# Kernel tuning notes

Measured on AMD Instinct MI355X. Metric: run time of the kernel, lower is better.

Reference implementation:

```python
import math
import jax, jax.numpy as jnp
import numpy as np

T, D, H = 2048, 2048, 16
C = D // H
EPS = 1e-6


def _rope_tables(c, t):
    inv_freq = 1.0 / (10000.0 ** (jnp.arange(0, c, 2, dtype=jnp.float32) / c))
    freqs = jnp.arange(t, dtype=jnp.float32)[:, None] * inv_freq[None, :]  # (T, C/2)
    return jnp.sin(freqs), jnp.cos(freqs)


def _rotate_every_two(x):
    x1 = x[..., ::2]
    x2 = x[..., 1::2]
    return jnp.stack((-x2, x1), axis=-1).reshape(x.shape)


def _apply_rope(x_htc, sin, cos):
    # sin/cos: (T, C/2) -> repeat each freq twice along channel -> (1, T, C)
    sin = jnp.repeat(sin, 2, axis=-1)[None]
    cos = jnp.repeat(cos, 2, axis=-1)[None]
    return x_htc * cos + _rotate_every_two(x_htc) * sin


def _layernorm(x, w):
    mu = jnp.mean(x, axis=-1, keepdims=True)
    var = jnp.var(x, axis=-1, keepdims=True)
    return (x - mu) / jnp.sqrt(var + EPS) * w


def setup_inputs() -> dict:
    key = jax.random.key(0)
    ks = jax.random.split(key, 4)
    x = jax.random.normal(ks[0], (T, D), dtype=jnp.float32)
    W_attn = jax.random.normal(ks[1], (3 * D, D), dtype=jnp.float32) * 0.02
    b_attn = jnp.zeros((3 * D,), dtype=jnp.float32)
    W_proj = jax.random.normal(ks[2], (D, D), dtype=jnp.float32) * 0.02
    b_proj = jnp.zeros((D,), dtype=jnp.float32)
    q_ln_w = jnp.ones((C,), dtype=jnp.float32)
    k_ln_w = jnp.ones((C,), dtype=jnp.float32)
    return {"x": x, "W_attn": W_attn, "b_attn": b_attn, "W_proj": W_proj,
            "b_proj": b_proj, "q_ln_w": q_ln_w, "k_ln_w": k_ln_w}


def reference(x, W_attn, b_attn, W_proj, b_proj, q_ln_w, k_ln_w):
    t, d = x.shape
    qkv = x @ W_attn.T + b_attn                      # (T, 3D)
    q, k, v = jnp.split(qkv, 3, axis=-1)
    q = q.reshape(t, H, C).transpose(1, 0, 2)        # (H, T, C)
    k = k.reshape(t, H, C).transpose(1, 0, 2)
    v = v.reshape(t, H, C).transpose(1, 0, 2)
    q = _layernorm(q, q_ln_w)
    k = _layernorm(k, k_ln_w)
    sin, cos = _rope_tables(C, t)
    q = _apply_rope(q, sin, cos)
    k = _apply_rope(k, sin, cos)
    a = jnp.einsum("htc,hsc->hts", q, k)             # (H, T, T)
    causal = jnp.tril(jnp.ones((1, t, t))) == 0
    a = jnp.where(causal, float("-inf"), a)
    scaling = math.sqrt(C)                            # q_ln active
    a = jax.nn.softmax(a.astype(jnp.float32) / scaling, axis=-1).astype(x.dtype)
    out = jnp.einsum("hts,hsc->htc", a, v)           # (H, T, C)
    out = out.transpose(1, 0, 2).reshape(t, d)       # (T, D)
    return out @ W_proj.T + b_proj
```

## Files before the change

### kernel.cpp

```cpp
#include <hip/hip_runtime.h>
#include <hip/hip_bf16.h>
#include <math.h>

#define T_DIM 2048
#define D_DIM 2048
#define H_DIM 16
#define C_DIM 128

typedef __bf16 bf16;
typedef __attribute__((ext_vector_type(8))) __bf16 bf16x8;
typedef __attribute__((ext_vector_type(4))) __bf16 bf16x4;
typedef __attribute__((ext_vector_type(2))) __bf16 bf16x2;
typedef __attribute__((ext_vector_type(4))) float f32x4;

__device__ __forceinline__ void gload_lds16(const void* g, void* l) {
  __builtin_amdgcn_global_load_lds((__attribute__((address_space(1))) void*)g,
                                   (__attribute__((address_space(3))) void*)l,
                                   16, 0, 0);
}

__global__ __launch_bounds__(256) void cvt3(
    const float* __restrict__ x, const float* __restrict__ wa, const float* __restrict__ wp,
    bf16* __restrict__ xo, bf16* __restrict__ wao, bf16* __restrict__ wpo)
{
  const int NX = 1048576, NA = 3145728;
  int i = blockIdx.x * 256 + threadIdx.x;
  for (; i < 5242880; i += 2048 * 256) {
    const float* s; bf16* d; int off;
    if (i < NX)            { s = x;  d = xo;  off = i; }
    else if (i < NX + NA)  { s = wa; d = wao; off = i - NX; }
    else                   { s = wp; d = wpo; off = i - NX - NA; }
    float4 v = reinterpret_cast<const float4*>(s)[off];
    bf16x4 o;
    o[0] = (bf16)v.x; o[1] = (bf16)v.y; o[2] = (bf16)v.z; o[3] = (bf16)v.w;
    reinterpret_cast<bf16x4*>(d)[off] = o;
  }
}

__global__ __launch_bounds__(512, 2) void gemm384_bt_bias(
    const bf16* __restrict__ A, const bf16* __restrict__ B,
    const float* __restrict__ bias, float* __restrict__ C,
    int M, int N, int K)
{
  __shared__ __align__(16) bf16 Asl[2][128 * 64];
  __shared__ __align__(16) bf16 Bsl[2][384 * 64];
  const int tid = threadIdx.x;
  const int lane = tid & 63;
  const int wv = tid >> 6;
  const int g = lane >> 4, r16 = lane & 15;
  const int wm = wv >> 2;
  const int wn = wv & 3;

  int bid = blockIdx.x;
  int bid2 = (bid & 7) * 32 + (bid >> 3);
  const int ntn = N / 384;
  const int bn = bid2 % ntn, bm = bid2 / ntn;

  const size_t Abase = (size_t)(bm * 128) * K;
  const size_t Bbase = (size_t)(bn * 384) * K;

  f32x4 acc[2][2][2][3] = {};
  bf16x8 a0[2][2], a1[2][2];
  bf16x8 b0[3][2], b1[3][2];

  auto stageA = [&](int bb, int t) {
#pragma unroll
    for (int i = 0; i < 2; ++i) {
      int c = i * 512 + tid;
      int r = c >> 3, p = c & 7, j = p ^ (r & 7);
      gload_lds16(A + Abase + (size_t)r * K + t * 64 + j * 8,
                  (char*)&Asl[bb][0] + (size_t)c * 16);
    }
  };
  auto stageB = [&](int bb, int u, int t) {
#pragma unroll
    for (int i = 0; i < 2; ++i) {
      int c = i * 512 + tid;
      int r = c >> 3, p = c & 7, j = p ^ (r & 7);
      gload_lds16(B + Bbase + (size_t)(u * 128 + r) * K + t * 64 + j * 8,
                  (char*)&Bsl[bb][0] + u * 16384 + (size_t)c * 16);
    }
  };
  auto readAh = [&](bf16x8 (&dst)[2][2], int bufi, int qr) {
#pragma unroll
    for (int R = 0; R < 2; ++R) {
      int ar = wm * 64 + qr * 32 + R * 16 + r16;
#pragma unroll
      for (int ks = 0; ks < 2; ++ks)
        dst[R][ks] = *reinterpret_cast<const bf16x8*>(
            &Asl[bufi][ar * 64 + (((ks * 4 + g) ^ (ar & 7)) << 3)]);
    }
  };
  auto readBh = [&](bf16x8 (&dst)[3][2], int bufi, int qc) {
#pragma unroll
    for (int F = 0; F < 3; ++F) {
      int br = wn * 96 + qc * 48 + F * 16 + r16;
#pragma unroll
      for (int ks = 0; ks < 2; ++ks)
        dst[F][ks] = *reinterpret_cast<const bf16x8*>(
            &Bsl[bufi][br * 64 + (((ks * 4 + g) ^ (br & 7)) << 3)]);
    }
  };
  auto mfma12 = [&](f32x4 (&cq)[2][3], bf16x8 (&aa)[2][2], bf16x8 (&bb)[3][2]) {
    __builtin_amdgcn_s_setprio(1);
#pragma unroll
    for (int ks = 0; ks < 2; ++ks)
#pragma unroll
      for (int R = 0; R < 2; ++R)
#pragma unroll
        for (int F = 0; F < 3; ++F)
          cq[R][F] = __builtin_amdgcn_mfma_f32_16x16x32_bf16(aa[R][ks], bb[F][ks], cq[R][F], 0, 0, 0);
    __builtin_amdgcn_s_setprio(0);
  };

#define PHASESYNC()                                               \
  __builtin_amdgcn_s_barrier();                                   \
  asm volatile("s_waitcnt lgkmcnt(0)" ::: "memory");              \
  __builtin_amdgcn_sched_barrier(0);

  stageA(0, 0); stageB(0, 0, 0); stageB(0, 1, 0); stageB(0, 2, 0);
  asm volatile("s_waitcnt vmcnt(0)" ::: "memory");
  __builtin_amdgcn_s_barrier();

  const int NT = K >> 6;
  for (int t = 0; t < NT; ++t) {
    const int cb = t & 1, nb = cb ^ 1;
    const bool pf = (t + 1 < NT);
    readAh(a0, cb, 0);
    readBh(b0, cb, 0);
    if (pf) { stageA(nb, t + 1); stageB(nb, 0, t + 1); }
    PHASESYNC()
    mfma12(acc[0][0], a0, b0);
    __builtin_amdgcn_s_barrier();
    readBh(b1, cb, 1);
    if (pf) stageB(nb, 1, t + 1);
    PHASESYNC()
    mfma12(acc[0][1], a0, b1);
    __builtin_amdgcn_s_barrier();
    readAh(a1, cb, 1);
    if (pf) stageB(nb, 2, t + 1);
    PHASESYNC()
    mfma12(acc[1][1], a1, b1);
    __builtin_amdgcn_s_barrier();
    mfma12(acc[1][0], a1, b0);
    asm volatile("s_waitcnt vmcnt(0)" ::: "memory");
    __builtin_amdgcn_s_barrier();
  }
#undef PHASESYNC

#pragma unroll
  for (int qr = 0; qr < 2; ++qr)
#pragma unroll
    for (int qc = 0; qc < 2; ++qc)
#pragma unroll
      for (int R = 0; R < 2; ++R)
#pragma unroll
        for (int F = 0; F < 3; ++F) {
          int row0 = bm * 128 + wm * 64 + qr * 32 + R * 16 + g * 4;
          int col  = bn * 384 + wn * 96 + qc * 48 + F * 16 + r16;
          float bv = bias[col];
#pragma unroll
          for (int rr = 0; rr < 4; ++rr)
            C[(size_t)(row0 + rr) * N + col] = acc[qr][qc][R][F][rr] + bv;
        }
}

__global__ __launch_bounds__(256) void gemm_bt_bias(
    const bf16* __restrict__ A, const bf16* __restrict__ B,
    const float* __restrict__ bias, float* __restrict__ C,
    int M, int N, int K)
{
  __shared__ __align__(16) bf16 As[2][128 * 32];
  __shared__ __align__(16) bf16 Bs[2][128 * 32];
  const int tid = threadIdx.x;
  const int lane = tid & 63;
  const int w = tid >> 6;
  const int wm = (w >> 1) * 64, wn = (w & 1) * 64;
  const int g = lane >> 4;
  const int r16 = lane & 15;
  const int bm = blockIdx.y, bn = blockIdx.x;

  f32x4 acc[4][4] = {};

  const size_t Abase = (size_t)(bm * 128) * K;
  const size_t Bbase = (size_t)(bn * 128) * K;

  auto stage = [&](int bb, int k0) {
#pragma unroll
    for (int c = 0; c < 2; ++c) {
      int e = c * 256 + tid;
      int row = e >> 2, col = (e & 3) * 8;
      gload_lds16(A + Abase + (size_t)row * K + k0 + col, (char*)&As[bb][0] + (size_t)e * 16);
      gload_lds16(B + Bbase + (size_t)row * K + k0 + col, (char*)&Bs[bb][0] + (size_t)e * 16);
    }
  };

  stage(0, 0);
  __syncthreads();

  for (int k0 = 0; k0 < K; k0 += 32) {
    const int cur = (k0 >> 5) & 1;
    if (k0 + 32 < K) stage(cur ^ 1, k0 + 32);
    bf16x8 a[4], b[4];
#pragma unroll
    for (int m = 0; m < 4; ++m)
      a[m] = *reinterpret_cast<const bf16x8*>(&As[cur][(wm + m * 16 + r16) * 32 + g * 8]);
#pragma unroll
    for (int n = 0; n < 4; ++n)
      b[n] = *reinterpret_cast<const bf16x8*>(&Bs[cur][(wn + n * 16 + r16) * 32 + g * 8]);
    __builtin_amdgcn_s_setprio(1);
#pragma unroll
    for (int m = 0; m < 4; ++m)
#pragma unroll
      for (int n = 0; n < 4; ++n)
        acc[m][n] = __builtin_amdgcn_mfma_f32_16x16x32_bf16(a[m], b[n], acc[m][n], 0, 0, 0);
    __builtin_amdgcn_s_setprio(0);
    __syncthreads();
  }

#pragma unroll
  for (int m = 0; m < 4; ++m) {
    int row0 = bm * 128 + wm + m * 16 + g * 4;
#pragma unroll
    for (int n = 0; n < 4; ++n) {
      int col = bn * 128 + wn + n * 16 + r16;
      float bv = bias[col];
#pragma unroll
      for (int rr = 0; rr < 4; ++rr)
        C[(size_t)(row0 + rr) * N + col] = acc[m][n][rr] + bv;
    }
  }
}

__global__ __launch_bounds__(256) void lnrope_vt_kernel(
    const float* __restrict__ qkv, const float* __restrict__ qw,
    const float* __restrict__ kw, bf16* __restrict__ qo, bf16* __restrict__ ko,
    bf16* __restrict__ vt)
{
  __shared__ bf16 tile[32][33];
  const int tid = threadIdx.x;
  if (blockIdx.x < 8192) {
    const int lane = tid & 63;
    const int wid = blockIdx.x * 4 + (tid >> 6);
    const int h = wid >> 11;
    const int t = wid & (T_DIM - 1);
    const int c0 = lane * 2;

    float inv_freq = exp2f(-13.287712379549449f * (float)c0 * (1.0f / 128.0f));
    float fr = (float)t * inv_freq;
    float sn = sinf(fr), cs = cosf(fr);
    const float scaleq = 0.08838834764831845f;

#pragma unroll
    for (int which = 0; which < 2; ++which) {
      const float* base = qkv + (size_t)t * (3 * D_DIM) + which * D_DIM + h * C_DIM;
      float2 v = *reinterpret_cast<const float2*>(base + c0);
      float s = v.x + v.y;
#pragma unroll
      for (int m = 32; m; m >>= 1) s += __shfl_xor(s, m);
      float mu = s * (1.0f / 128.0f);
      float d0 = v.x - mu, d1 = v.y - mu;
      float ss = d0 * d0 + d1 * d1;
#pragma unroll
      for (int m = 32; m; m >>= 1) ss += __shfl_xor(ss, m);
      float rstd = rsqrtf(ss * (1.0f / 128.0f) + 1e-6f);
      const float* wgt = which ? kw : qw;
      float x0 = d0 * rstd * wgt[c0], x1 = d1 * rstd * wgt[c0 + 1];
      float o0 = x0 * cs - x1 * sn;
      float o1 = x1 * cs + x0 * sn;
      if (!which) { o0 *= scaleq; o1 *= scaleq; }
      bf16* out = (which ? ko : qo) + ((size_t)h * T_DIM + t) * C_DIM + c0;
      bf16x2 ob; ob[0] = (bf16)o0; ob[1] = (bf16)o1;
      *reinterpret_cast<bf16x2*>(out) = ob;
    }
  } else {
    const int vb = blockIdx.x - 8192;
    const int t0 = (vb & 63) * 32;
    const int c0 = ((vb >> 6) & 3) * 32;
    const int h = vb >> 8;
    const int tx = tid & 31, ty = tid >> 5;
#pragma unroll
    for (int i = 0; i < 4; ++i) {
      int t = t0 + ty + i * 8;
      tile[ty + i * 8][tx] =
          (bf16)qkv[(size_t)t * (3 * D_DIM) + 2 * D_DIM + h * C_DIM + c0 + tx];
    }
    __syncthreads();
#pragma unroll
    for (int i = 0; i < 4; ++i) {
      int c = c0 + ty + i * 8;
      vt[((size_t)h * C_DIM + c) * T_DIM + t0 + tx] = tile[tx][ty + i * 8];
    }
  }
}

__global__ __launch_bounds__(256, 4) void attn_kernel(
    const bf16* __restrict__ Q, const bf16* __restrict__ K,
    const bf16* __restrict__ VT, bf16* __restrict__ AO,
    float* __restrict__ U, float* __restrict__ ML)
{
  __shared__ __align__(16) bf16 Ks[2][32 * 128];
  __shared__ __align__(16) bf16 Vs[2][128 * 32];
  __shared__ __align__(16) bf16 p_lds[4][16 * 32];
  const int tid = threadIdx.x;
  const int lane = tid & 63;
  const int w = tid >> 6;
  const int g = lane >> 4, r16 = lane & 15;
  const int h = blockIdx.y;
  const int b = blockIdx.x;

  int qb, kb0, kb1, sp;
  if (b < 32) { qb = 16 + (b >> 1); sp = b & 1; kb0 = sp * 32; kb1 = sp ? (2 * qb + 2) : 32; }
  else        { qb = 47 - b;        sp = -1;    kb0 = 0;       kb1 = 2 * qb + 2; }
  const int qr0 = qb * 64 + w * 16;
  const int qrow = qr0 + r16;

  const bf16* Qh = Q + (size_t)h * T_DIM * C_DIM;
  const bf16* Kh = K + (size_t)h * T_DIM * C_DIM;
  const bf16* Vh = VT + (size_t)h * C_DIM * T_DIM;

  bf16x8 qf[4];
#pragma unroll
  for (int kk = 0; kk < 4; ++kk)
    qf[kk] = *reinterpret_cast<const bf16x8*>(
        &Qh[(size_t)qrow * C_DIM + kk * 32 + g * 8]);

  float mrow = -INFINITY, lrow = 0.f;
  f32x4 o[8] = {};

  auto stage = [&](int bb, int kb) {
    const bf16* Kt = Kh + (size_t)(kb * 32) * C_DIM;
    const bf16* Vt = Vh + kb * 32;
#pragma unroll
    for (int i = 0; i < 2; ++i) {
      int e = i * 256 + tid;
      int r = e >> 4, p = e & 15, j = p ^ (r & 7);
      gload_lds16(Kt + r * C_DIM + j * 8, (char*)&Ks[bb][0] + (size_t)e * 16);
    }
#pragma unroll
    for (int i = 0; i < 2; ++i) {
      int e = i * 256 + tid;
      int r = e >> 2, p = e & 3, j = p ^ ((r >> 1) & 3);
      gload_lds16(Vt + (size_t)r * T_DIM + j * 8, (char*)&Vs[bb][0] + (size_t)e * 16);
    }
  };

  stage(0, kb0);
  __syncthreads();
  int buf = 0;

  for (int kb = kb0; kb < kb1; ++kb) {
    if (kb + 1 < kb1) stage(buf ^ 1, kb + 1);

    f32x4 sacc[2] = {};
    __builtin_amdgcn_s_setprio(1);
#pragma unroll
    for (int n = 0; n < 2; ++n) {
      int kr = n * 16 + r16;
      const bf16* kbase = &Ks[buf][kr << 7];
#pragma unroll
      for (int kk = 0; kk < 4; ++kk) {
        bf16x8 kf = *reinterpret_cast<const bf16x8*>(
            kbase + (((kk * 4 + g) ^ (kr & 7)) << 3));
        sacc[n] = __builtin_amdgcn_mfma_f32_16x16x32_bf16(kf, qf[kk], sacc[n], 0, 0, 0);
      }
    }
    __builtin_amdgcn_s_setprio(0);
    if (kb * 32 + 31 > qr0) {
#pragma unroll
      for (int n = 0; n < 2; ++n)
#pragma unroll
        for (int rr = 0; rr < 4; ++rr)
          if (kb * 32 + n * 16 + g * 4 + rr > qrow) sacc[n][rr] = -3.0e38f;
    }
    float mx = fmaxf(fmaxf(fmaxf(sacc[0][0], sacc[0][1]), fmaxf(sacc[0][2], sacc[0][3])),
                     fmaxf(fmaxf(sacc[1][0], sacc[1][1]), fmaxf(sacc[1][2], sacc[1][3])));
    mx = fmaxf(mx, __shfl_xor(mx, 16));
    mx = fmaxf(mx, __shfl_xor(mx, 32));
    float alpha = 1.0f;
    bool need = __any(mx > mrow + 8.0f);
    if (need) {
      float mnew = fmaxf(mrow, mx);
      alpha = __expf(mrow - mnew);
      mrow = mnew;
    }
    float ps = 0.f;
#pragma unroll
    for (int n = 0; n < 2; ++n)
#pragma unroll
      for (int rr = 0; rr < 4; ++rr) {
        float p = __expf(sacc[n][rr] - mrow);
        sacc[n][rr] = p;
        ps += p;
      }
    ps += __shfl_xor(ps, 16);
    ps += __shfl_xor(ps, 32);
    lrow = lrow * alpha + ps;
    if (need) {
#pragma unroll
      for (int nc = 0; nc < 8; ++nc)
#pragma unroll
        for (int rr = 0; rr < 4; ++rr)
          o[nc][rr] *= alpha;
    }
    {
      bf16* prow = &p_lds[w][r16 << 5];
      const int ssw = (r16 >> 1) & 3;
#pragma unroll
      for (int n = 0; n < 2; ++n) {
        bf16x4 pk;
        pk[0] = (bf16)sacc[n][0]; pk[1] = (bf16)sacc[n][1];
        pk[2] = (bf16)sacc[n][2]; pk[3] = (bf16)sacc[n][3];
        int c8 = 2 * n + (g >> 1);
        *reinterpret_cast<bf16x4*>(prow + (((c8 ^ ssw) << 3) | ((g & 1) << 2))) = pk;
      }
    }
    asm volatile("s_waitcnt lgkmcnt(0)" ::: "memory");
    __builtin_amdgcn_s_setprio(1);
    bf16x8 pf = *reinterpret_cast<const bf16x8*>(
        &p_lds[w][(r16 << 5) + ((g ^ ((r16 >> 1) & 3)) << 3)]);
#pragma unroll
    for (int nc = 0; nc < 8; ++nc) {
      int vr = nc * 16 + r16;
      bf16x8 vf = *reinterpret_cast<const bf16x8*>(
          &Vs[buf][(vr << 5) + ((g ^ ((vr >> 1) & 3)) << 3)]);
      o[nc] = __builtin_amdgcn_mfma_f32_16x16x32_bf16(vf, pf, o[nc], 0, 0, 0);
    }
    __builtin_amdgcn_s_setprio(0);
    __syncthreads();
    buf ^= 1;
  }

  if (sp < 0) {
    float inv = 1.0f / lrow;
    bf16* arow = &AO[(size_t)qrow * D_DIM + h * C_DIM + (g << 2)];
#pragma unroll
    for (int nc = 0; nc < 8; ++nc) {
      bf16x4 ob;
      ob[0] = (bf16)(o[nc][0] * inv); ob[1] = (bf16)(o[nc][1] * inv);
      ob[2] = (bf16)(o[nc][2] * inv); ob[3] = (bf16)(o[nc][3] * inv);
      *reinterpret_cast<bf16x4*>(arow + nc * 16) = ob;
    }
  } else {
    const int qi = qb - 16;
    const size_t ubase = ((size_t)(h * 16 + qi) * 2 + sp) * (64 * 128);
    const size_t mlbase = (size_t)(h * 16 + qi) * 256 + sp * 128;
    const int row = w * 16 + r16;
    float* urow = &U[ubase + (size_t)row * 128 + (g << 2)];
#pragma unroll
    for (int nc = 0; nc < 8; ++nc)
      *reinterpret_cast<f32x4*>(urow + nc * 16) = o[nc];
    if (g == 0) {
      ML[mlbase + row] = mrow;
      ML[mlbase + 64 + row] = lrow;
    }
  }
}

__global__ __launch_bounds__(256) void attn_combine(
    const float* __restrict__ U, const float* __restrict__ ML, bf16* __restrict__ AO)
{
  int idx = blockIdx.x * 256 + threadIdx.x;
  int c4 = (idx & 31) * 4;
  int r = idx >> 5;
  int trow = r & 63;
  int qi = (r >> 6) & 15;
  int h = r >> 10;

  size_t mlbase = (size_t)(h * 16 + qi) * 256;
  float m0 = ML[mlbase + trow],       l0 = ML[mlbase + 64 + trow];
  float m1 = ML[mlbase + 128 + trow], l1 = ML[mlbase + 192 + trow];
  float m = fmaxf(m0, m1);
  float a0 = __expf(m0 - m), a1 = __expf(m1 - m);
  float inv = 1.0f / (l0 * a0 + l1 * a1);

  size_t t0 = ((size_t)(h * 16 + qi) * 2) * (64 * 128) + (size_t)trow * 128 + c4;
  float4 u0 = *reinterpret_cast<const float4*>(U + t0);
  float4 u1 = *reinterpret_cast<const float4*>(U + t0 + 64 * 128);
  int t = 1024 + qi * 64 + trow;
  bf16x4 ob;
  ob[0] = (bf16)((u0.x * a0 + u1.x * a1) * inv);
  ob[1] = (bf16)((u0.y * a0 + u1.y * a1) * inv);
  ob[2] = (bf16)((u0.z * a0 + u1.z * a1) * inv);
  ob[3] = (bf16)((u0.w * a0 + u1.w * a1) * inv);
  *reinterpret_cast<bf16x4*>(&AO[(size_t)t * D_DIM + h * C_DIM + c4]) = ob;
}

extern "C" void kernel_launch(void* const* d_in, const int* in_sizes, int n_in,
                              void* d_out, int out_size, void* d_ws, size_t ws_size,
                              hipStream_t stream)
{
  const float* x      = (const float*)d_in[0];
  const float* W_attn = (const float*)d_in[1];
  const float* b_attn = (const float*)d_in[2];
  const float* W_proj = (const float*)d_in[3];
  const float* b_proj = (const float*)d_in[4];
  const float* q_ln_w = (const float*)d_in[5];
  const float* k_ln_w = (const float*)d_in[6];

  char* ws = (char*)d_ws;
  bf16*  x_bf  = (bf16*)(ws + 0);
  bf16*  wa_bf = (bf16*)(ws + 8388608);
  bf16*  wp_bf = (bf16*)(ws + 33554432);
  float* qkv   = (float*)(ws + 41943040);
  bf16*  q_bf  = (bf16*)(ws + 92274688);
  bf16*  k_bf  = (bf16*)(ws + 100663296);
  bf16*  vt    = (bf16*)(ws + 109051904);
  bf16*  ao    = (bf16*)(ws + 117440512);
  float* U  = (float*)(ws + 41943040);
  float* ML = (float*)(ws + 58720256);

  cvt3<<<2048, 256, 0, stream>>>(x, W_attn, W_proj, x_bf, wa_bf, wp_bf);

  gemm384_bt_bias<<<dim3((T_DIM / 128) * (3 * D_DIM / 384)), dim3(512), 0, stream>>>(
      x_bf, wa_bf, b_attn, qkv, T_DIM, 3 * D_DIM, D_DIM);

  lnrope_vt_kernel<<<8192 + 4096, 256, 0, stream>>>(qkv, q_ln_w, k_ln_w, q_bf, k_bf, vt);

  attn_kernel<<<dim3(48, H_DIM), 256, 0, stream>>>(q_bf, k_bf, vt, ao, U, ML);
  attn_combine<<<2048, 256, 0, stream>>>(U, ML, ao);

  gemm_bt_bias<<<dim3(D_DIM / 128, T_DIM / 128), 256, 0, stream>>>(
      ao, wp_bf, b_proj, (float*)d_out, T_DIM, D_DIM, D_DIM);
}
```

Baseline: 187.7 us.

## Store QKV as bf16, simplify QKV GEMM pipeline, retile output projection GEMM

The QKV GEMM now writes bf16 instead of fp32, which halves the intermediate traffic written by the GEMM and read back by the LayerNorm/RoPE/V-transpose kernel. The U and ML buffers move to new workspace offsets so they no longer overlap the QKV region. The QKV GEMM's phased barrier/prefetch schedule and setprio hints are replaced by a simpler single prefetch per K-step followed by all MFMAs. The output-projection GEMM moves to a 64-deep K tile with swizzled LDS, block-index remapping and two blocks per CU. Rounding QKV to bf16 before LayerNorm adds some precision loss, and the simpler schedule may overlap loads and compute less well.

Result: faster. 170.3 us (-9.3%).

```diff
diff --git a/kernel.cpp b/kernel.cpp
--- a/kernel.cpp
+++ b/kernel.cpp
@@ -37,9 +37,10 @@
   }
 }
 
+template <typename OutT>
 __global__ __launch_bounds__(512, 2) void gemm384_bt_bias(
     const bf16* __restrict__ A, const bf16* __restrict__ B,
-    const float* __restrict__ bias, float* __restrict__ C,
+    const float* __restrict__ bias, OutT* __restrict__ C,
     int M, int N, int K)
 {
   __shared__ __align__(16) bf16 Asl[2][128 * 64];
@@ -52,7 +53,7 @@
   const int wn = wv & 3;
 
   int bid = blockIdx.x;
-  int bid2 = (bid & 7) * 32 + (bid >> 3);
+  int bid2 = (bid & 7) * (gridDim.x >> 3) + (bid >> 3);
   const int ntn = N / 384;
   const int bn = bid2 % ntn, bm = bid2 / ntn;
 
@@ -102,7 +103,6 @@
     }
   };
   auto mfma12 = [&](f32x4 (&cq)[2][3], bf16x8 (&aa)[2][2], bf16x8 (&bb)[3][2]) {
-    __builtin_amdgcn_s_setprio(1);
 #pragma unroll
     for (int ks = 0; ks < 2; ++ks)
 #pragma unroll
@@ -110,43 +110,25 @@
 #pragma unroll
         for (int F = 0; F < 3; ++F)
           cq[R][F] = __builtin_amdgcn_mfma_f32_16x16x32_bf16(aa[R][ks], bb[F][ks], cq[R][F], 0, 0, 0);
-    __builtin_amdgcn_s_setprio(0);
-  };
-
-#define PHASESYNC()                                               \
-  __builtin_amdgcn_s_barrier();                                   \
-  asm volatile("s_waitcnt lgkmcnt(0)" ::: "memory");              \
-  __builtin_amdgcn_sched_barrier(0);
+  };
 
   stageA(0, 0); stageB(0, 0, 0); stageB(0, 1, 0); stageB(0, 2, 0);
-  asm volatile("s_waitcnt vmcnt(0)" ::: "memory");
-  __builtin_amdgcn_s_barrier();
+  __syncthreads();
 
   const int NT = K >> 6;
   for (int t = 0; t < NT; ++t) {
     const int cb = t & 1, nb = cb ^ 1;
-    const bool pf = (t + 1 < NT);
-    readAh(a0, cb, 0);
-    readBh(b0, cb, 0);
-    if (pf) { stageA(nb, t + 1); stageB(nb, 0, t + 1); }
-    PHASESYNC()
+    if (t + 1 < NT) {
+      stageA(nb, t + 1); stageB(nb, 0, t + 1); stageB(nb, 1, t + 1); stageB(nb, 2, t + 1);
+    }
+    readAh(a0, cb, 0); readAh(a1, cb, 1);
+    readBh(b0, cb, 0); readBh(b1, cb, 1);
     mfma12(acc[0][0], a0, b0);
-    __builtin_amdgcn_s_barrier();
-    readBh(b1, cb, 1);
-    if (pf) stageB(nb, 1, t + 1);
-    PHASESYNC()
     mfma12(acc[0][1], a0, b1);
-    __builtin_amdgcn_s_barrier();
-    readAh(a1, cb, 1);
-    if (pf) stageB(nb, 2, t + 1);
-    PHASESYNC()
     mfma12(acc[1][1], a1, b1);
-    __builtin_amdgcn_s_barrier();
     mfma12(acc[1][0], a1, b0);
-    asm volatile("s_waitcnt vmcnt(0)" ::: "memory");
-    __builtin_amdgcn_s_barrier();
-  }
-#undef PHASESYNC
+    __syncthreads();
+  }
 
 #pragma unroll
   for (int qr = 0; qr < 2; ++qr)
@@ -161,60 +143,77 @@
           float bv = bias[col];
 #pragma unroll
           for (int rr = 0; rr < 4; ++rr)
-            C[(size_t)(row0 + rr) * N + col] = acc[qr][qc][R][F][rr] + bv;
+            C[(size_t)(row0 + rr) * N + col] = (OutT)(acc[qr][qc][R][F][rr] + bv);
         }
 }
 
-__global__ __launch_bounds__(256) void gemm_bt_bias(
+__global__ __launch_bounds__(256, 2) void gemm_bt_bias(
     const bf16* __restrict__ A, const bf16* __restrict__ B,
     const float* __restrict__ bias, float* __restrict__ C,
     int M, int N, int K)
 {
-  __shared__ __align__(16) bf16 As[2][128 * 32];
-  __shared__ __align__(16) bf16 Bs[2][128 * 32];
+  __shared__ __align__(16) bf16 As[2][128 * 64];
+  __shared__ __align__(16) bf16 Bs[2][128 * 64];
   const int tid = threadIdx.x;
   const int lane = tid & 63;
   const int w = tid >> 6;
   const int wm = (w >> 1) * 64, wn = (w & 1) * 64;
   const int g = lane >> 4;
   const int r16 = lane & 15;
-  const int bm = blockIdx.y, bn = blockIdx.x;
+
+  int lb = blockIdx.y * gridDim.x + blockIdx.x;
+  int nblk = gridDim.x * gridDim.y;
+  int s = (lb & 7) * (nblk >> 3) + (lb >> 3);
+  const int bn = s % gridDim.x, bm = s / gridDim.x;
 
   f32x4 acc[4][4] = {};
 
   const size_t Abase = (size_t)(bm * 128) * K;
   const size_t Bbase = (size_t)(bn * 128) * K;
 
-  auto stage = [&](int bb, int k0) {
-#pragma unroll
-    for (int c = 0; c < 2; ++c) {
-      int e = c * 256 + tid;
-      int row = e >> 2, col = (e & 3) * 8;
-      gload_lds16(A + Abase + (size_t)row * K + k0 + col, (char*)&As[bb][0] + (size_t)e * 16);
-      gload_lds16(B + Bbase + (size_t)row * K + k0 + col, (char*)&Bs[bb][0] + (size_t)e * 16);
+  auto stage = [&](int bb, int t) {
+#pragma unroll
+    for (int i = 0; i < 4; ++i) {
+      int c = i * 256 + tid;
+      int r = c >> 3, p = c & 7, j = p ^ (r & 7);
+      gload_lds16(A + Abase + (size_t)r * K + t * 64 + j * 8,
+                  (char*)&As[bb][0] + (size_t)c * 16);
+      gload_lds16(B + Bbase + (size_t)r * K + t * 64 + j * 8,
+                  (char*)&Bs[bb][0] + (size_t)c * 16);
     }
   };
 
   stage(0, 0);
   __syncthreads();
 
-  for (int k0 = 0; k0 < K; k0 += 32) {
-    const int cur = (k0 >> 5) & 1;
-    if (k0 + 32 < K) stage(cur ^ 1, k0 + 32);
-    bf16x8 a[4], b[4];
-#pragma unroll
-    for (int m = 0; m < 4; ++m)
-      a[m] = *reinterpret_cast<const bf16x8*>(&As[cur][(wm + m * 16 + r16) * 32 + g * 8]);
-#pragma unroll
-    for (int n = 0; n < 4; ++n)
-      b[n] = *reinterpret_cast<const bf16x8*>(&Bs[cur][(wn + n * 16 + r16) * 32 + g * 8]);
-    __builtin_amdgcn_s_setprio(1);
-#pragma unroll
-    for (int m = 0; m < 4; ++m)
-#pragma unroll
-      for (int n = 0; n < 4; ++n)
-        acc[m][n] = __builtin_amdgcn_mfma_f32_16x16x32_bf16(a[m], b[n], acc[m][n], 0, 0, 0);
-    __builtin_amdgcn_s_setprio(0);
+  const int NT = K >> 6;
+  for (int t = 0; t < NT; ++t) {
+    const int cb = t & 1, nb = cb ^ 1;
+    if (t + 1 < NT) stage(nb, t + 1);
+    bf16x8 a[4][2], b[4][2];
+#pragma unroll
+    for (int m = 0; m < 4; ++m) {
+      int ar = wm + m * 16 + r16;
+#pragma unroll
+      for (int ks = 0; ks < 2; ++ks)
+        a[m][ks] = *reinterpret_cast<const bf16x8*>(
+            &As[cb][ar * 64 + (((ks * 4 + g) ^ (ar & 7)) << 3)]);
+    }
+#pragma unroll
+    for (int n = 0; n < 4; ++n) {
+      int br = wn + n * 16 + r16;
+#pragma unroll
+      for (int ks = 0; ks < 2; ++ks)
+        b[n][ks] = *reinterpret_cast<const bf16x8*>(
+            &Bs[cb][br * 64 + (((ks * 4 + g) ^ (br & 7)) << 3)]);
+    }
+#pragma unroll
+    for (int ks = 0; ks < 2; ++ks)
+#pragma unroll
+      for (int m = 0; m < 4; ++m)
+#pragma unroll
+        for (int n = 0; n < 4; ++n)
+          acc[m][n] = __builtin_amdgcn_mfma_f32_16x16x32_bf16(a[m][ks], b[n][ks], acc[m][n], 0, 0, 0);
     __syncthreads();
   }
 
@@ -233,7 +232,7 @@
 }
 
 __global__ __launch_bounds__(256) void lnrope_vt_kernel(
-    const float* __restrict__ qkv, const float* __restrict__ qw,
+    const bf16* __restrict__ qkv, const float* __restrict__ qw,
     const float* __restrict__ kw, bf16* __restrict__ qo, bf16* __restrict__ ko,
     bf16* __restrict__ vt)
 {
@@ -253,13 +252,14 @@
 
 #pragma unroll
     for (int which = 0; which < 2; ++which) {
-      const float* base = qkv + (size_t)t * (3 * D_DIM) + which * D_DIM + h * C_DIM;
-      float2 v = *reinterpret_cast<const float2*>(base + c0);
-      float s = v.x + v.y;
+      const bf16* base = qkv + (size_t)t * (3 * D_DIM) + which * D_DIM + h * C_DIM;
+      bf16x2 v2 = *reinterpret_cast<const bf16x2*>(base + c0);
+      float vx = (float)v2[0], vy = (float)v2[1];
+      float s = vx + vy;
 #pragma unroll
       for (int m = 32; m; m >>= 1) s += __shfl_xor(s, m);
       float mu = s * (1.0f / 128.0f);
-      float d0 = v.x - mu, d1 = v.y - mu;
+      float d0 = vx - mu, d1 = vy - mu;
       float ss = d0 * d0 + d1 * d1;
 #pragma unroll
       for (int m = 32; m; m >>= 1) ss += __shfl_xor(ss, m);
@@ -283,7 +283,7 @@
     for (int i = 0; i < 4; ++i) {
       int t = t0 + ty + i * 8;
       tile[ty + i * 8][tx] =
-          (bf16)qkv[(size_t)t * (3 * D_DIM) + 2 * D_DIM + h * C_DIM + c0 + tx];
+          qkv[(size_t)t * (3 * D_DIM) + 2 * D_DIM + h * C_DIM + c0 + tx];
     }
     __syncthreads();
 #pragma unroll
@@ -502,17 +502,17 @@
   bf16*  x_bf  = (bf16*)(ws + 0);
   bf16*  wa_bf = (bf16*)(ws + 8388608);
   bf16*  wp_bf = (bf16*)(ws + 33554432);
-  float* qkv   = (float*)(ws + 41943040);
+  bf16*  qkv   = (bf16*)(ws + 41943040);
+  float* U     = (float*)(ws + 67108864);
+  float* ML    = (float*)(ws + 83886080);
   bf16*  q_bf  = (bf16*)(ws + 92274688);
   bf16*  k_bf  = (bf16*)(ws + 100663296);
   bf16*  vt    = (bf16*)(ws + 109051904);
   bf16*  ao    = (bf16*)(ws + 117440512);
-  float* U  = (float*)(ws + 41943040);
-  float* ML = (float*)(ws + 58720256);
 
   cvt3<<<2048, 256, 0, stream>>>(x, W_attn, W_proj, x_bf, wa_bf, wp_bf);
 
-  gemm384_bt_bias<<<dim3((T_DIM / 128) * (3 * D_DIM / 384)), dim3(512), 0, stream>>>(
+  gemm384_bt_bias<bf16><<<dim3((T_DIM / 128) * (3 * D_DIM / 384)), dim3(512), 0, stream>>>(
       x_bf, wa_bf, b_attn, qkv, T_DIM, 3 * D_DIM, D_DIM);
 
   lnrope_vt_kernel<<<8192 + 4096, 256, 0, stream>>>(qkv, q_ln_w, k_ln_w, q_bf, k_bf, vt);
```
